# Kernel tuning notes

Hardware: AMD Instinct MI355X
Metric: run time of the kernel (lower is better)

## Reference

```python
import jax, jax.numpy as jnp
import numpy as np

D, H, W = 16, 16, 16          # token grid = img_size/patch_size at i_layer=0
NUM_HEADS = 8
DISTANCE = 10.0               # 10 - i_layer


def _local_pattern(d, h, w, distance):
    # faithful to local_nd_pattern: meshgrid (ij), flatten, cdist p=2, < distance
    g = jnp.meshgrid(jnp.arange(d), jnp.arange(h), jnp.arange(w), indexing='ij')
    coords = jnp.stack([c.reshape(-1) for c in g], axis=1).astype(jnp.float32)  # [N,3]
    diff = coords[:, None, :] - coords[None, :, :]                               # [N,N,3]
    dist = jnp.sqrt(jnp.sum(diff * diff, axis=-1))
    return dist < distance                                                       # [N,N] bool


def setup_inputs() -> dict:
    key = jax.random.key(0)
    k1, k2, k3 = jax.random.split(key, 3)
    dim = 256
    x = jax.random.normal(k1, (1, dim, D, H, W), dtype=jnp.float32)
    qkv_w = jax.random.normal(k2, (3 * dim, dim), dtype=jnp.float32) * (dim ** -0.5)
    proj_w = jax.random.normal(k3, (dim, dim), dtype=jnp.float32) * (dim ** -0.5)
    proj_b = jnp.zeros((dim,), dtype=jnp.float32)
    return {"x": x, "qkv_w": qkv_w, "proj_w": proj_w, "proj_b": proj_b}


def reference(x, qkv_w, proj_w, proj_b):
    b, c, d, h, w = x.shape
    n = d * h * w
    hd = c // NUM_HEADS
    mask = _local_pattern(d, h, w, DISTANCE)                  # [N,N] bool

    # b c d h w -> b (dhw) c
    tok = x.reshape(b, c, n).transpose(0, 2, 1)               # [B,N,C]
    qkv = jnp.einsum('bnc,oc->bno', tok, qkv_w)               # [B,N,3C]
    qkv = qkv.reshape(b, n, 3, NUM_HEADS, hd)
    qkv = qkv.transpose(2, 0, 3, 1, 4)                        # [3,B,H,N,hd]
    q, k, v = qkv[0], qkv[1], qkv[2]                          # [B,H,N,hd]

    scale = 1.0 / jnp.sqrt(jnp.asarray(hd, dtype=x.dtype))
    scores = jnp.einsum('bhnd,bhmd->bhnm', q, k) * scale      # [B,H,N,N]
    scores = jnp.where(mask[None, None], scores, -jnp.inf)
    attn = jax.nn.softmax(scores, axis=-1)
    out = jnp.einsum('bhnm,bhmd->bhnd', attn, v)              # [B,H,N,hd]

    out = out.transpose(0, 2, 1, 3).reshape(b, n, c)          # [B,N,C]
    out = jnp.einsum('bnc,oc->bno', out, proj_w) + proj_b
    # b (dhw) c -> b c d h w
    out = out.transpose(0, 2, 1).reshape(b, c, d, h, w)
    return out
```

## Files before the change

### kernel.cpp

```cpp
#include <hip/hip_runtime.h>
#include <hip/hip_bf16.h>

typedef __attribute__((ext_vector_type(8))) short short8;
typedef __attribute__((ext_vector_type(4))) float floatx4;

#define L2E 1.4426950408889634f

#if __has_builtin(__builtin_amdgcn_exp2f)
#define EXP2(x) __builtin_amdgcn_exp2f(x)
#else
#define EXP2(x) exp2f(x)
#endif
#if __has_builtin(__builtin_amdgcn_rcpf)
#define RCP(x) __builtin_amdgcn_rcpf(x)
#else
#define RCP(x) (1.0f / (x))
#endif

static __device__ __forceinline__ unsigned short f2bf(float f) {
    unsigned int u = __builtin_bit_cast(unsigned int, f);
    u += 0x7fffu + ((u >> 16) & 1u);
    return (unsigned short)(u >> 16);
}
static __device__ __forceinline__ unsigned int pk_bf16(float a, float b) {
    __hip_bfloat162 h2 = __float22bfloat162_rn(make_float2(a, b));
    unsigned int u;
    __builtin_memcpy(&u, &h2, 4);
    return u;
}

__global__ __launch_bounds__(256) void k_qkv(const float* __restrict__ x,
                                             const float* __restrict__ qw,
                                             unsigned short* __restrict__ qm,
                                             unsigned short* __restrict__ km,
                                             unsigned short* __restrict__ vt) {
    __shared__ __align__(16) unsigned short At[64][136];
    __shared__ __align__(16) unsigned short Wt[64][136];
    const int tid = threadIdx.x;
    const int wave = tid >> 6, lane = tid & 63;
    const int l16 = lane & 15, quad = lane >> 4;
    const int m0 = blockIdx.x * 64;
    const int o0 = blockIdx.y * 64;

    floatx4 acc[4] = {};
    for (int rnd = 0; rnd < 2; ++rnd) {
        const int cbase = rnd * 128;
        if (rnd) __syncthreads();
        {
            const int moff = (tid & 3) * 16;
            #pragma unroll
            for (int half = 0; half < 2; ++half) {
                const int c_l = (tid >> 2) + 64 * half;
                const float4* xp = reinterpret_cast<const float4*>(
                    x + (size_t)(cbase + c_l) * 4096 + m0 + moff);
                const float4 f0 = xp[0], f1 = xp[1], f2 = xp[2], f3 = xp[3];
                At[moff +  0][c_l] = f2bf(f0.x); At[moff +  1][c_l] = f2bf(f0.y);
                At[moff +  2][c_l] = f2bf(f0.z); At[moff +  3][c_l] = f2bf(f0.w);
                At[moff +  4][c_l] = f2bf(f1.x); At[moff +  5][c_l] = f2bf(f1.y);
                At[moff +  6][c_l] = f2bf(f1.z); At[moff +  7][c_l] = f2bf(f1.w);
                At[moff +  8][c_l] = f2bf(f2.x); At[moff +  9][c_l] = f2bf(f2.y);
                At[moff + 10][c_l] = f2bf(f2.z); At[moff + 11][c_l] = f2bf(f2.w);
                At[moff + 12][c_l] = f2bf(f3.x); At[moff + 13][c_l] = f2bf(f3.y);
                At[moff + 14][c_l] = f2bf(f3.z); At[moff + 15][c_l] = f2bf(f3.w);
            }
        }
        {
            const int o_l = tid >> 2, cp = (tid & 3) * 32;
            const float4* wp = reinterpret_cast<const float4*>(
                qw + (size_t)(o0 + o_l) * 256 + cbase + cp);
            #pragma unroll
            for (int j = 0; j < 2; ++j) {
                const float4 g0 = wp[4 * j + 0], g1 = wp[4 * j + 1];
                const float4 g2 = wp[4 * j + 2], g3 = wp[4 * j + 3];
                unsigned int u[8];
                u[0] = pk_bf16(g0.x, g0.y); u[1] = pk_bf16(g0.z, g0.w);
                u[2] = pk_bf16(g1.x, g1.y); u[3] = pk_bf16(g1.z, g1.w);
                u[4] = pk_bf16(g2.x, g2.y); u[5] = pk_bf16(g2.z, g2.w);
                u[6] = pk_bf16(g3.x, g3.y); u[7] = pk_bf16(g3.z, g3.w);
                __builtin_memcpy(&Wt[o_l][cp + 16 * j], u, 32);
            }
        }
        __syncthreads();
        #pragma unroll
        for (int cc = 0; cc < 4; ++cc) {
            const int c0 = cc * 32 + quad * 8;
            const short8 a = *reinterpret_cast<const short8*>(&At[wave * 16 + l16][c0]);
            #pragma unroll
            for (int t4 = 0; t4 < 4; ++t4) {
                const short8 b = *reinterpret_cast<const short8*>(&Wt[t4 * 16 + l16][c0]);
                acc[t4] = __builtin_amdgcn_mfma_f32_16x16x32_bf16(a, b, acc[t4], 0, 0, 0);
            }
        }
    }
    const float qscale = 0.17677669529663687f * L2E;
    #pragma unroll
    for (int t4 = 0; t4 < 4; ++t4) {
        #pragma unroll
        for (int r = 0; r < 4; ++r) {
            const int n = m0 + wave * 16 + quad * 4 + r;
            const int o = o0 + t4 * 16 + l16;
            const int s = o >> 8, rem = o & 255, head = rem >> 5, t = rem & 31;
            if (s == 0)       qm[((size_t)head * 4096 + n) * 32 + t] = f2bf(acc[t4][r] * qscale);
            else if (s == 1)  km[((size_t)head * 4096 + n) * 32 + t] = f2bf(acc[t4][r]);
            else              vt[((size_t)head * 32 + t) * 4096 + n] = f2bf(acc[t4][r]);
        }
    }
}

__global__ __launch_bounds__(256, 2) void k_attn(const unsigned short* __restrict__ qm,
                                                 const unsigned short* __restrict__ km,
                                                 const unsigned short* __restrict__ vt,
                                                 unsigned short* __restrict__ ao) {
    const int h   = blockIdx.y;
    const int nq0 = blockIdx.x * 64;
    const int tid = threadIdx.x;
    const int wv  = tid >> 6;
    const int lane = tid & 63;
    const int l16 = lane & 15, quad = lane >> 4;
    const int nqw = nq0 + wv * 16;

    __shared__ __align__(16) unsigned short Kt[2][2048];
    __shared__ __align__(16) unsigned short Vt[2][2048];
    __shared__ __align__(16) unsigned short PT[4][16][72];

    const short8 a_q = *reinterpret_cast<const short8*>(
        qm + ((size_t)h * 4096 + nqw + l16) * 32 + quad * 8);

    const int hq = (nqw >> 4) & 15;
    const int dq = nq0 >> 8;
    float dw2[4];
    #pragma unroll
    for (int r = 0; r < 4; ++r) {
        const float dw = (float)(quad * 4 + r - l16);
        dw2[r] = dw * dw;
    }

    const int dk_lo = (dq > 9) ? dq - 9 : 0;
    const int dk_hi = (dq < 6) ? dq + 9 : 15;
    const int NT = 4 * (dk_hi - dk_lo + 1);

    const int skey = tid >> 2;
    const int sdo  = (tid & 3) * 8;
    const int sdim = tid >> 3;
    const int skg  = tid & 7;
    const unsigned short* ksrc = km + ((size_t)h << 17) + skey * 32 + sdo;
    const unsigned short* vsrc = vt + (((size_t)h * 32 + sdim) << 12) + skg * 8;
    const int kdst = (skey * 32 + sdo) ^ ((skey & 7) << 3);
    const int vdst = (skg * 256 + sdim * 8) ^ (skg << 3);

    float l_acc = 0.f;
    floatx4 o_acc[2] = {};

#define J0T(T) (((dk_lo + ((T) >> 2)) << 8) + (((T) & 3) << 6))

    short8 gK, gV;
    {
        const int j0 = J0T(0);
        gK = *reinterpret_cast<const short8*>(ksrc + (size_t)j0 * 32);
        gV = *reinterpret_cast<const short8*>(vsrc + j0);
        *reinterpret_cast<short8*>(&Kt[0][kdst]) = gK;
        *reinterpret_cast<short8*>(&Vt[0][vdst]) = gV;
        const int j1 = J0T(1);
        gK = *reinterpret_cast<const short8*>(ksrc + (size_t)j1 * 32);
        gV = *reinterpret_cast<const short8*>(vsrc + j1);
    }
    __syncthreads();

    for (int t = 0; t < NT; ++t) {
        const int cb = t & 1, nb = cb ^ 1;

        *reinterpret_cast<short8*>(&Kt[nb][kdst]) = gK;
        *reinterpret_cast<short8*>(&Vt[nb][vdst]) = gV;

        {
            const int tn = (t + 2 < NT) ? t + 2 : NT - 1;
            const int j2 = J0T(tn);
            gK = *reinterpret_cast<const short8*>(ksrc + (size_t)j2 * 32);
            gV = *reinterpret_cast<const short8*>(vsrc + j2);
        }

        {
            const int dk = dk_lo + (t >> 2), g = t & 3;
            const int dd = dq - dk;
            const int bb = 100 - dd * dd;
            const int h0 = hq - 4 * g;
            int thr[4];
            thr[0] = bb - h0 * h0;
            thr[1] = bb - (h0 - 1) * (h0 - 1);
            thr[2] = bb - (h0 - 2) * (h0 - 2);
            thr[3] = bb - (h0 - 3) * (h0 - 3);

            if (thr[0] > 0 || thr[1] > 0 || thr[2] > 0 || thr[3] > 0) {
                #pragma unroll
                for (int t4 = 0; t4 < 4; ++t4) {
                    const bool sib = (thr[t4 ^ 1] > 0);
                    if (thr[t4] > 0) {
                        const short8 kf = *reinterpret_cast<const short8*>(
                            &Kt[cb][((t4 * 16 + l16) * 32 + quad * 8) ^ ((l16 & 7) << 3)]);
                        const floatx4 sf = __builtin_amdgcn_mfma_f32_16x16x32_bf16(
                            kf, a_q, (floatx4){0.f, 0.f, 0.f, 0.f}, 0, 0, 0);
                        const float thrf = (float)thr[t4];
                        const float p0 = (dw2[0] < thrf) ? EXP2(sf[0]) : 0.f;
                        const float p1 = (dw2[1] < thrf) ? EXP2(sf[1]) : 0.f;
                        const float p2 = (dw2[2] < thrf) ? EXP2(sf[2]) : 0.f;
                        const float p3 = (dw2[3] < thrf) ? EXP2(sf[3]) : 0.f;
                        l_acc += (p0 + p1) + (p2 + p3);
                        unsigned int pair[2];
                        pair[0] = pk_bf16(p0, p1);
                        pair[1] = pk_bf16(p2, p3);
                        __builtin_memcpy(&PT[wv][l16][t4 * 16 + quad * 4], pair, 8);
                    } else if (sib) {
                        const unsigned int zz[2] = {0u, 0u};
                        __builtin_memcpy(&PT[wv][l16][t4 * 16 + quad * 4], zz, 8);
                    }
                }
                #pragma unroll
                for (int kt = 0; kt < 2; ++kt) {
                    if (thr[2 * kt] > 0 || thr[2 * kt + 1] > 0) {
                        const short8 b_p = *reinterpret_cast<const short8*>(
                            &PT[wv][l16][kt * 32 + quad * 8]);
                        const int kg = kt * 4 + quad;
                        #pragma unroll
                        for (int hf = 0; hf < 2; ++hf) {
                            const short8 vf = *reinterpret_cast<const short8*>(
                                &Vt[cb][(kg * 256 + (hf * 16 + l16) * 8) ^ (kg << 3)]);
                            o_acc[hf] = __builtin_amdgcn_mfma_f32_16x16x32_bf16(
                                vf, b_p, o_acc[hf], 0, 0, 0);
                        }
                    }
                }
            }
        }
        __syncthreads();
    }
#undef J0T

    l_acc += __shfl_xor(l_acc, 16);
    l_acc += __shfl_xor(l_acc, 32);
    const float inv = RCP(l_acc);
    #pragma unroll
    for (int hf = 0; hf < 2; ++hf) {
        unsigned int uu[2];
        uu[0] = pk_bf16(o_acc[hf][0] * inv, o_acc[hf][1] * inv);
        uu[1] = pk_bf16(o_acc[hf][2] * inv, o_acc[hf][3] * inv);
        __builtin_memcpy(ao + (size_t)(nqw + l16) * 256 + h * 32 + hf * 16 + quad * 4,
                         uu, 8);
    }
}

__global__ __launch_bounds__(256) void k_proj(const unsigned short* __restrict__ ao,
                                              const float* __restrict__ pw,
                                              const float* __restrict__ pb,
                                              float* __restrict__ out) {
    __shared__ __align__(16) unsigned short Pt[64][264];
    const int tid = threadIdx.x;
    const int wave = tid >> 6, lane = tid & 63;
    const int l16 = lane & 15, quad = lane >> 4;
    const int n0 = blockIdx.x * 64;
    const int m0 = blockIdx.y * 64;

    {
        const int o_l = tid >> 2, cp = (tid & 3) * 64;
        const float4* wp = reinterpret_cast<const float4*>(pw + (size_t)(m0 + o_l) * 256 + cp);
        #pragma unroll
        for (int j = 0; j < 4; ++j) {
            const float4 g0 = wp[4 * j + 0], g1 = wp[4 * j + 1];
            const float4 g2 = wp[4 * j + 2], g3 = wp[4 * j + 3];
            unsigned int u[8];
            u[0] = pk_bf16(g0.x, g0.y); u[1] = pk_bf16(g0.z, g0.w);
            u[2] = pk_bf16(g1.x, g1.y); u[3] = pk_bf16(g1.z, g1.w);
            u[4] = pk_bf16(g2.x, g2.y); u[5] = pk_bf16(g2.z, g2.w);
            u[6] = pk_bf16(g3.x, g3.y); u[7] = pk_bf16(g3.z, g3.w);
            __builtin_memcpy(&Pt[o_l][cp + 16 * j], u, 32);
        }
    }
    __syncthreads();

    floatx4 acc[4] = {};
    #pragma unroll
    for (int cc = 0; cc < 8; ++cc) {
        const int c0 = cc * 32 + quad * 8;
        const short8 a = *reinterpret_cast<const short8*>(&Pt[wave * 16 + l16][c0]);
        #pragma unroll
        for (int t4 = 0; t4 < 4; ++t4) {
            const short8 b = *reinterpret_cast<const short8*>(
                ao + (size_t)(n0 + t4 * 16 + l16) * 256 + c0);
            acc[t4] = __builtin_amdgcn_mfma_f32_16x16x32_bf16(a, b, acc[t4], 0, 0, 0);
        }
    }
    #pragma unroll
    for (int t4 = 0; t4 < 4; ++t4) {
        #pragma unroll
        for (int r = 0; r < 4; ++r) {
            const int o = m0 + wave * 16 + quad * 4 + r;
            const int n = n0 + t4 * 16 + l16;
            out[(size_t)o * 4096 + n] = acc[t4][r] + pb[o];
        }
    }
}

extern "C" void kernel_launch(void* const* d_in, const int* in_sizes, int n_in,
                              void* d_out, int out_size, void* d_ws, size_t ws_size,
                              hipStream_t stream) {
    const float* x      = (const float*)d_in[0];
    const float* qkv_w  = (const float*)d_in[1];
    const float* proj_w = (const float*)d_in[2];
    const float* proj_b = (const float*)d_in[3];
    float* out = (float*)d_out;

    char* B = (char*)d_ws;
    const size_t MB = 1u << 20;
    unsigned short* ao = (unsigned short*)(B);
    unsigned short* qm = (unsigned short*)(B + 2 * MB);
    unsigned short* km = (unsigned short*)(B + 4 * MB);
    unsigned short* vt = (unsigned short*)(B + 6 * MB);

    k_qkv<<<dim3(64, 12), 256, 0, stream>>>(x, qkv_w, qm, km, vt);
    k_attn<<<dim3(64, 8), 256, 0, stream>>>(qm, km, vt, ao);
    k_proj<<<dim3(64, 4), 256, 0, stream>>>(ao, proj_w, proj_b, out);
}
```

Baseline: 152.0 us.

## Process two key tiles per barrier with split accumulators and swizzled P buffer

The attention loop now stages two 64-key K/V tiles per iteration, so there is one __syncthreads for every two tiles instead of one per tile. It also keeps two independent output accumulators, letting MFMA chains from the two tiles interleave, and XOR-swizzles the per-wave P scratch to cut LDS bank conflicts. In exchange it doubles the LDS footprint and register pressure for the prefetch and accumulator state, which may lower occupancy. The tile-count parity is not guarded, but NT is always a multiple of 4, so the two-tile stride is safe.

```diff
diff --git a/kernel.cpp b/kernel.cpp
--- a/kernel.cpp
+++ b/kernel.cpp
@@ -119,9 +119,9 @@
     const int l16 = lane & 15, quad = lane >> 4;
     const int nqw = nq0 + wv * 16;
 
-    __shared__ __align__(16) unsigned short Kt[2][2048];
-    __shared__ __align__(16) unsigned short Vt[2][2048];
-    __shared__ __align__(16) unsigned short PT[4][16][72];
+    __shared__ __align__(16) unsigned short Kt[2][2][2048];
+    __shared__ __align__(16) unsigned short Vt[2][2][2048];
+    __shared__ __align__(16) unsigned short PT[4][2][16][72];
 
     const short8 a_q = *reinterpret_cast<const short8*>(
         qm + ((size_t)h * 4096 + nqw + l16) * 32 + quad * 8);
@@ -147,90 +147,104 @@
     const unsigned short* vsrc = vt + (((size_t)h * 32 + sdim) << 12) + skg * 8;
     const int kdst = (skey * 32 + sdo) ^ ((skey & 7) << 3);
     const int vdst = (skg * 256 + sdim * 8) ^ (skg << 3);
+    const int ptswz = (l16 & 7) << 3;
 
     float l_acc = 0.f;
-    floatx4 o_acc[2] = {};
+    floatx4 o_acc[2][2] = {};
 
 #define J0T(T) (((dk_lo + ((T) >> 2)) << 8) + (((T) & 3) << 6))
 
-    short8 gK, gV;
+    auto comp = [&](int T, int cbuf, int sl) {
+        const int dk = dk_lo + (T >> 2), g = T & 3;
+        const int dd = dq - dk;
+        const int bb = 100 - dd * dd;
+        const int h0 = hq - 4 * g;
+        int thr[4];
+        thr[0] = bb - h0 * h0;
+        thr[1] = bb - (h0 - 1) * (h0 - 1);
+        thr[2] = bb - (h0 - 2) * (h0 - 2);
+        thr[3] = bb - (h0 - 3) * (h0 - 3);
+        if (!(thr[0] > 0 || thr[1] > 0 || thr[2] > 0 || thr[3] > 0)) return;
+
+        #pragma unroll
+        for (int t4 = 0; t4 < 4; ++t4) {
+            const bool sib = (thr[t4 ^ 1] > 0);
+            if (thr[t4] > 0) {
+                const short8 kf = *reinterpret_cast<const short8*>(
+                    &Kt[cbuf][sl][((t4 * 16 + l16) * 32 + quad * 8) ^ ((l16 & 7) << 3)]);
+                const floatx4 sf = __builtin_amdgcn_mfma_f32_16x16x32_bf16(
+                    kf, a_q, (floatx4){0.f, 0.f, 0.f, 0.f}, 0, 0, 0);
+                const float thrf = (float)thr[t4];
+                const float p0 = (dw2[0] < thrf) ? EXP2(sf[0]) : 0.f;
+                const float p1 = (dw2[1] < thrf) ? EXP2(sf[1]) : 0.f;
+                const float p2 = (dw2[2] < thrf) ? EXP2(sf[2]) : 0.f;
+                const float p3 = (dw2[3] < thrf) ? EXP2(sf[3]) : 0.f;
+                l_acc += (p0 + p1) + (p2 + p3);
+                unsigned int pair[2];
+                pair[0] = pk_bf16(p0, p1);
+                pair[1] = pk_bf16(p2, p3);
+                __builtin_memcpy(&PT[wv][sl][l16][(t4 * 16 + quad * 4) ^ ptswz], pair, 8);
+            } else if (sib) {
+                const unsigned int zz[2] = {0u, 0u};
+                __builtin_memcpy(&PT[wv][sl][l16][(t4 * 16 + quad * 4) ^ ptswz], zz, 8);
+            }
+        }
+        #pragma unroll
+        for (int kt = 0; kt < 2; ++kt) {
+            if (thr[2 * kt] > 0 || thr[2 * kt + 1] > 0) {
+                const short8 b_p = *reinterpret_cast<const short8*>(
+                    &PT[wv][sl][l16][(kt * 32 + quad * 8) ^ ptswz]);
+                const int kg = kt * 4 + quad;
+                #pragma unroll
+                for (int hf = 0; hf < 2; ++hf) {
+                    const short8 vf = *reinterpret_cast<const short8*>(
+                        &Vt[cbuf][sl][(kg * 256 + (hf * 16 + l16) * 8) ^ (kg << 3)]);
+                    o_acc[sl][hf] = __builtin_amdgcn_mfma_f32_16x16x32_bf16(
+                        vf, b_p, o_acc[sl][hf], 0, 0, 0);
+                }
+            }
+        }
+    };
+
+    short8 gK0, gV0, gK1, gV1;
     {
-        const int j0 = J0T(0);
-        gK = *reinterpret_cast<const short8*>(ksrc + (size_t)j0 * 32);
-        gV = *reinterpret_cast<const short8*>(vsrc + j0);
-        *reinterpret_cast<short8*>(&Kt[0][kdst]) = gK;
-        *reinterpret_cast<short8*>(&Vt[0][vdst]) = gV;
-        const int j1 = J0T(1);
-        gK = *reinterpret_cast<const short8*>(ksrc + (size_t)j1 * 32);
-        gV = *reinterpret_cast<const short8*>(vsrc + j1);
+        const int ja = J0T(0), jb = J0T(1);
+        const short8 k0 = *reinterpret_cast<const short8*>(ksrc + (size_t)ja * 32);
+        const short8 v0 = *reinterpret_cast<const short8*>(vsrc + ja);
+        const short8 k1 = *reinterpret_cast<const short8*>(ksrc + (size_t)jb * 32);
+        const short8 v1 = *reinterpret_cast<const short8*>(vsrc + jb);
+        *reinterpret_cast<short8*>(&Kt[0][0][kdst]) = k0;
+        *reinterpret_cast<short8*>(&Vt[0][0][vdst]) = v0;
+        *reinterpret_cast<short8*>(&Kt[0][1][kdst]) = k1;
+        *reinterpret_cast<short8*>(&Vt[0][1][vdst]) = v1;
+        const int jc = J0T(2), jd = J0T(3);
+        gK0 = *reinterpret_cast<const short8*>(ksrc + (size_t)jc * 32);
+        gV0 = *reinterpret_cast<const short8*>(vsrc + jc);
+        gK1 = *reinterpret_cast<const short8*>(ksrc + (size_t)jd * 32);
+        gV1 = *reinterpret_cast<const short8*>(vsrc + jd);
     }
     __syncthreads();
 
-    for (int t = 0; t < NT; ++t) {
-        const int cb = t & 1, nb = cb ^ 1;
-
-        *reinterpret_cast<short8*>(&Kt[nb][kdst]) = gK;
-        *reinterpret_cast<short8*>(&Vt[nb][vdst]) = gV;
+    for (int t2 = 0; t2 < NT; t2 += 2) {
+        const int cb = (t2 >> 1) & 1, nb = cb ^ 1;
+
+        *reinterpret_cast<short8*>(&Kt[nb][0][kdst]) = gK0;
+        *reinterpret_cast<short8*>(&Vt[nb][0][vdst]) = gV0;
+        *reinterpret_cast<short8*>(&Kt[nb][1][kdst]) = gK1;
+        *reinterpret_cast<short8*>(&Vt[nb][1][vdst]) = gV1;
 
         {
-            const int tn = (t + 2 < NT) ? t + 2 : NT - 1;
-            const int j2 = J0T(tn);
-            gK = *reinterpret_cast<const short8*>(ksrc + (size_t)j2 * 32);
-            gV = *reinterpret_cast<const short8*>(vsrc + j2);
-        }
-
-        {
-            const int dk = dk_lo + (t >> 2), g = t & 3;
-            const int dd = dq - dk;
-            const int bb = 100 - dd * dd;
-            const int h0 = hq - 4 * g;
-            int thr[4];
-            thr[0] = bb - h0 * h0;
-            thr[1] = bb - (h0 - 1) * (h0 - 1);
-            thr[2] = bb - (h0 - 2) * (h0 - 2);
-            thr[3] = bb - (h0 - 3) * (h0 - 3);
-
-            if (thr[0] > 0 || thr[1] > 0 || thr[2] > 0 || thr[3] > 0) {
-                #pragma unroll
-                for (int t4 = 0; t4 < 4; ++t4) {
-                    const bool sib = (thr[t4 ^ 1] > 0);
-                    if (thr[t4] > 0) {
-                        const short8 kf = *reinterpret_cast<const short8*>(
-                            &Kt[cb][((t4 * 16 + l16) * 32 + quad * 8) ^ ((l16 & 7) << 3)]);
-                        const floatx4 sf = __builtin_amdgcn_mfma_f32_16x16x32_bf16(
-                            kf, a_q, (floatx4){0.f, 0.f, 0.f, 0.f}, 0, 0, 0);
-                        const float thrf = (float)thr[t4];
-                        const float p0 = (dw2[0] < thrf) ? EXP2(sf[0]) : 0.f;
-                        const float p1 = (dw2[1] < thrf) ? EXP2(sf[1]) : 0.f;
-                        const float p2 = (dw2[2] < thrf) ? EXP2(sf[2]) : 0.f;
-                        const float p3 = (dw2[3] < thrf) ? EXP2(sf[3]) : 0.f;
-                        l_acc += (p0 + p1) + (p2 + p3);
-                        unsigned int pair[2];
-                        pair[0] = pk_bf16(p0, p1);
-                        pair[1] = pk_bf16(p2, p3);
-                        __builtin_memcpy(&PT[wv][l16][t4 * 16 + quad * 4], pair, 8);
-                    } else if (sib) {
-                        const unsigned int zz[2] = {0u, 0u};
-                        __builtin_memcpy(&PT[wv][l16][t4 * 16 + quad * 4], zz, 8);
-                    }
-                }
-                #pragma unroll
-                for (int kt = 0; kt < 2; ++kt) {
-                    if (thr[2 * kt] > 0 || thr[2 * kt + 1] > 0) {
-                        const short8 b_p = *reinterpret_cast<const short8*>(
-                            &PT[wv][l16][kt * 32 + quad * 8]);
-                        const int kg = kt * 4 + quad;
-                        #pragma unroll
-                        for (int hf = 0; hf < 2; ++hf) {
-                            const short8 vf = *reinterpret_cast<const short8*>(
-                                &Vt[cb][(kg * 256 + (hf * 16 + l16) * 8) ^ (kg << 3)]);
-                            o_acc[hf] = __builtin_amdgcn_mfma_f32_16x16x32_bf16(
-                                vf, b_p, o_acc[hf], 0, 0, 0);
-                        }
-                    }
-                }
-            }
-        }
+            int ta = t2 + 4; if (ta >= NT) ta = NT - 1;
+            int tb = t2 + 5; if (tb >= NT) tb = NT - 1;
+            const int ja = J0T(ta), jb = J0T(tb);
+            gK0 = *reinterpret_cast<const short8*>(ksrc + (size_t)ja * 32);
+            gV0 = *reinterpret_cast<const short8*>(vsrc + ja);
+            gK1 = *reinterpret_cast<const short8*>(ksrc + (size_t)jb * 32);
+            gV1 = *reinterpret_cast<const short8*>(vsrc + jb);
+        }
+
+        comp(t2, cb, 0);
+        comp(t2 + 1, cb, 1);
         __syncthreads();
     }
 #undef J0T
@@ -240,9 +254,10 @@
     const float inv = RCP(l_acc);
     #pragma unroll
     for (int hf = 0; hf < 2; ++hf) {
+        const floatx4 os = o_acc[0][hf] + o_acc[1][hf];
         unsigned int uu[2];
-        uu[0] = pk_bf16(o_acc[hf][0] * inv, o_acc[hf][1] * inv);
-        uu[1] = pk_bf16(o_acc[hf][2] * inv, o_acc[hf][3] * inv);
+        uu[0] = pk_bf16(os[0] * inv, os[1] * inv);
+        uu[1] = pk_bf16(os[2] * inv, os[3] * inv);
         __builtin_memcpy(ao + (size_t)(nqw + l16) * 256 + h * 32 + hf * 16 + quad * 4,
                          uu, 8);
     }
```

Result: slower. 163.4 us (+7.5%).

## Halve attention block to two waves and restructure K/V prefetch pipeline

Applied to the files above, without the earlier changes.

The attention kernel now uses 128-thread blocks covering 32 queries each, launching twice as many blocks, with each thread loading two K and two V vectors per tile. The prefetch schedule changes from a two-tiles-ahead register stage to one tile ahead: global loads are issued before compute and written to the other LDS buffer after it. This aims to raise block count and occupancy (launch bounds 128,4) and to hide load latency behind the tile's compute. The trade-off is that each block amortises its K/V tile loads over fewer queries, so total global/LDS traffic per query doubles.

```diff
diff --git a/kernel.cpp b/kernel.cpp
--- a/kernel.cpp
+++ b/kernel.cpp
@@ -107,12 +107,12 @@
     }
 }
 
-__global__ __launch_bounds__(256, 2) void k_attn(const unsigned short* __restrict__ qm,
+__global__ __launch_bounds__(128, 4) void k_attn(const unsigned short* __restrict__ qm,
                                                  const unsigned short* __restrict__ km,
                                                  const unsigned short* __restrict__ vt,
                                                  unsigned short* __restrict__ ao) {
     const int h   = blockIdx.y;
-    const int nq0 = blockIdx.x * 64;
+    const int nq0 = blockIdx.x * 32;
     const int tid = threadIdx.x;
     const int wv  = tid >> 6;
     const int lane = tid & 63;
@@ -121,7 +121,7 @@
 
     __shared__ __align__(16) unsigned short Kt[2][2048];
     __shared__ __align__(16) unsigned short Vt[2][2048];
-    __shared__ __align__(16) unsigned short PT[4][16][72];
+    __shared__ __align__(16) unsigned short PT[2][16][72];
 
     const short8 a_q = *reinterpret_cast<const short8*>(
         qm + ((size_t)h * 4096 + nqw + l16) * 32 + quad * 8);
@@ -139,100 +139,103 @@
     const int dk_hi = (dq < 6) ? dq + 9 : 15;
     const int NT = 4 * (dk_hi - dk_lo + 1);
 
-    const int skey = tid >> 2;
-    const int sdo  = (tid & 3) * 8;
-    const int sdim = tid >> 3;
-    const int skg  = tid & 7;
-    const unsigned short* ksrc = km + ((size_t)h << 17) + skey * 32 + sdo;
-    const unsigned short* vsrc = vt + (((size_t)h * 32 + sdim) << 12) + skg * 8;
-    const int kdst = (skey * 32 + sdo) ^ ((skey & 7) << 3);
-    const int vdst = (skg * 256 + sdim * 8) ^ (skg << 3);
+    const int skey = tid >> 2, sdo = (tid & 3) * 8;
+    const unsigned short* ksrcA = km + ((size_t)h << 17) + skey * 32 + sdo;
+    const unsigned short* ksrcB = ksrcA + 32 * 32;
+    const int kdA = (skey * 32 + sdo) ^ ((skey & 7) << 3);
+    const int kdB = kdA + 1024;
+    const int skg = tid & 7, sdim = tid >> 3;
+    const unsigned short* vsrcA = vt + (((size_t)h * 32 + sdim) << 12) + skg * 8;
+    const unsigned short* vsrcB = vsrcA + (16 << 12);
+    const int vdA = (skg * 256 + sdim * 8) ^ (skg << 3);
+    const int vdB = vdA + 128;
 
     float l_acc = 0.f;
     floatx4 o_acc[2] = {};
 
 #define J0T(T) (((dk_lo + ((T) >> 2)) << 8) + (((T) & 3) << 6))
 
-    short8 gK, gV;
-    {
-        const int j0 = J0T(0);
-        gK = *reinterpret_cast<const short8*>(ksrc + (size_t)j0 * 32);
-        gV = *reinterpret_cast<const short8*>(vsrc + j0);
-        *reinterpret_cast<short8*>(&Kt[0][kdst]) = gK;
-        *reinterpret_cast<short8*>(&Vt[0][vdst]) = gV;
-        const int j1 = J0T(1);
-        gK = *reinterpret_cast<const short8*>(ksrc + (size_t)j1 * 32);
-        gV = *reinterpret_cast<const short8*>(vsrc + j1);
-    }
+    auto comp = [&](int T, int cbuf) {
+        const int dk = dk_lo + (T >> 2), g = T & 3;
+        const int dd = dq - dk;
+        const int bb = 100 - dd * dd;
+        const int h0 = hq - 4 * g;
+        int thr[4];
+        thr[0] = bb - h0 * h0;
+        thr[1] = bb - (h0 - 1) * (h0 - 1);
+        thr[2] = bb - (h0 - 2) * (h0 - 2);
+        thr[3] = bb - (h0 - 3) * (h0 - 3);
+        if (!(thr[0] > 0 || thr[1] > 0 || thr[2] > 0 || thr[3] > 0)) return;
+
+        #pragma unroll
+        for (int t4 = 0; t4 < 4; ++t4) {
+            const bool sib = (thr[t4 ^ 1] > 0);
+            if (thr[t4] > 0) {
+                const short8 kf = *reinterpret_cast<const short8*>(
+                    &Kt[cbuf][((t4 * 16 + l16) * 32 + quad * 8) ^ ((l16 & 7) << 3)]);
+                const floatx4 sf = __builtin_amdgcn_mfma_f32_16x16x32_bf16(
+                    kf, a_q, (floatx4){0.f, 0.f, 0.f, 0.f}, 0, 0, 0);
+                const float thrf = (float)thr[t4];
+                const float p0 = (dw2[0] < thrf) ? EXP2(sf[0]) : 0.f;
+                const float p1 = (dw2[1] < thrf) ? EXP2(sf[1]) : 0.f;
+                const float p2 = (dw2[2] < thrf) ? EXP2(sf[2]) : 0.f;
+                const float p3 = (dw2[3] < thrf) ? EXP2(sf[3]) : 0.f;
+                l_acc += (p0 + p1) + (p2 + p3);
+                unsigned int pair[2];
+                pair[0] = pk_bf16(p0, p1);
+                pair[1] = pk_bf16(p2, p3);
+                __builtin_memcpy(&PT[wv][l16][t4 * 16 + quad * 4], pair, 8);
+            } else if (sib) {
+                const unsigned int zz[2] = {0u, 0u};
+                __builtin_memcpy(&PT[wv][l16][t4 * 16 + quad * 4], zz, 8);
+            }
+        }
+        #pragma unroll
+        for (int kt = 0; kt < 2; ++kt) {
+            if (thr[2 * kt] > 0 || thr[2 * kt + 1] > 0) {
+                const short8 b_p = *reinterpret_cast<const short8*>(
+                    &PT[wv][l16][kt * 32 + quad * 8]);
+                const int kg = kt * 4 + quad;
+                #pragma unroll
+                for (int hf = 0; hf < 2; ++hf) {
+                    const short8 vf = *reinterpret_cast<const short8*>(
+                        &Vt[cbuf][(kg * 256 + (hf * 16 + l16) * 8) ^ (kg << 3)]);
+                    o_acc[hf] = __builtin_amdgcn_mfma_f32_16x16x32_bf16(
+                        vf, b_p, o_acc[hf], 0, 0, 0);
+                }
+            }
+        }
+    };
+
+    short8 rK0, rK1, rV0, rV1;
+#define LOADT(T) {                                                        \
+        const int j0_ = J0T(T);                                           \
+        rK0 = *reinterpret_cast<const short8*>(ksrcA + (size_t)j0_ * 32); \
+        rK1 = *reinterpret_cast<const short8*>(ksrcB + (size_t)j0_ * 32); \
+        rV0 = *reinterpret_cast<const short8*>(vsrcA + j0_);              \
+        rV1 = *reinterpret_cast<const short8*>(vsrcB + j0_);              \
+    }
+#define WRITET(NB) {                                                      \
+        *reinterpret_cast<short8*>(&Kt[NB][kdA]) = rK0;                   \
+        *reinterpret_cast<short8*>(&Kt[NB][kdB]) = rK1;                   \
+        *reinterpret_cast<short8*>(&Vt[NB][vdA]) = rV0;                   \
+        *reinterpret_cast<short8*>(&Vt[NB][vdB]) = rV1;                   \
+    }
+
+    LOADT(0)
+    WRITET(0)
     __syncthreads();
 
     for (int t = 0; t < NT; ++t) {
         const int cb = t & 1, nb = cb ^ 1;
-
-        *reinterpret_cast<short8*>(&Kt[nb][kdst]) = gK;
-        *reinterpret_cast<short8*>(&Vt[nb][vdst]) = gV;
-
-        {
-            const int tn = (t + 2 < NT) ? t + 2 : NT - 1;
-            const int j2 = J0T(tn);
-            gK = *reinterpret_cast<const short8*>(ksrc + (size_t)j2 * 32);
-            gV = *reinterpret_cast<const short8*>(vsrc + j2);
-        }
-
-        {
-            const int dk = dk_lo + (t >> 2), g = t & 3;
-            const int dd = dq - dk;
-            const int bb = 100 - dd * dd;
-            const int h0 = hq - 4 * g;
-            int thr[4];
-            thr[0] = bb - h0 * h0;
-            thr[1] = bb - (h0 - 1) * (h0 - 1);
-            thr[2] = bb - (h0 - 2) * (h0 - 2);
-            thr[3] = bb - (h0 - 3) * (h0 - 3);
-
-            if (thr[0] > 0 || thr[1] > 0 || thr[2] > 0 || thr[3] > 0) {
-                #pragma unroll
-                for (int t4 = 0; t4 < 4; ++t4) {
-                    const bool sib = (thr[t4 ^ 1] > 0);
-                    if (thr[t4] > 0) {
-                        const short8 kf = *reinterpret_cast<const short8*>(
-                            &Kt[cb][((t4 * 16 + l16) * 32 + quad * 8) ^ ((l16 & 7) << 3)]);
-                        const floatx4 sf = __builtin_amdgcn_mfma_f32_16x16x32_bf16(
-                            kf, a_q, (floatx4){0.f, 0.f, 0.f, 0.f}, 0, 0, 0);
-                        const float thrf = (float)thr[t4];
-                        const float p0 = (dw2[0] < thrf) ? EXP2(sf[0]) : 0.f;
-                        const float p1 = (dw2[1] < thrf) ? EXP2(sf[1]) : 0.f;
-                        const float p2 = (dw2[2] < thrf) ? EXP2(sf[2]) : 0.f;
-                        const float p3 = (dw2[3] < thrf) ? EXP2(sf[3]) : 0.f;
-                        l_acc += (p0 + p1) + (p2 + p3);
-                        unsigned int pair[2];
-                        pair[0] = pk_bf16(p0, p1);
-                        pair[1] = pk_bf16(p2, p3);
-                        __builtin_memcpy(&PT[wv][l16][t4 * 16 + quad * 4], pair, 8);
-                    } else if (sib) {
-                        const unsigned int zz[2] = {0u, 0u};
-                        __builtin_memcpy(&PT[wv][l16][t4 * 16 + quad * 4], zz, 8);
-                    }
-                }
-                #pragma unroll
-                for (int kt = 0; kt < 2; ++kt) {
-                    if (thr[2 * kt] > 0 || thr[2 * kt + 1] > 0) {
-                        const short8 b_p = *reinterpret_cast<const short8*>(
-                            &PT[wv][l16][kt * 32 + quad * 8]);
-                        const int kg = kt * 4 + quad;
-                        #pragma unroll
-                        for (int hf = 0; hf < 2; ++hf) {
-                            const short8 vf = *reinterpret_cast<const short8*>(
-                                &Vt[cb][(kg * 256 + (hf * 16 + l16) * 8) ^ (kg << 3)]);
-                            o_acc[hf] = __builtin_amdgcn_mfma_f32_16x16x32_bf16(
-                                vf, b_p, o_acc[hf], 0, 0, 0);
-                        }
-                    }
-                }
-            }
-        }
+        const int tn = (t + 1 < NT) ? t + 1 : t;
+        LOADT(tn)
+        comp(t, cb);
+        WRITET(nb)
         __syncthreads();
     }
+#undef WRITET
+#undef LOADT
 #undef J0T
 
     l_acc += __shfl_xor(l_acc, 16);
@@ -316,6 +319,6 @@
     unsigned short* vt = (unsigned short*)(B + 6 * MB);
 
     k_qkv<<<dim3(64, 12), 256, 0, stream>>>(x, qkv_w, qm, km, vt);
-    k_attn<<<dim3(64, 8), 256, 0, stream>>>(qm, km, vt, ao);
+    k_attn<<<dim3(128, 8), 128, 0, stream>>>(qm, km, vt, ao);
     k_proj<<<dim3(64, 4), 256, 0, stream>>>(ao, proj_w, proj_b, out);
 }
```

After: 154.3 us. No clear change (+1.6%).
